# Kernel optimization log

Measured on AMD Instinct MI355X. Metric: run time of the kernel, lower is better.

## Reference

```python
import jax, jax.numpy as jnp
import numpy as np

N = 8192
D_IN = 1024
D_OUT = 1024


def setup_inputs() -> dict:
    key = jax.random.key(0)
    k0, k1, k2, k3 = jax.random.split(key, 4)
    scale = 1.0 / np.sqrt(D_IN)  # roughly matches nn.Linear init magnitude
    return {
        "x": jax.random.normal(k0, (N, D_IN), dtype=jnp.float32),
        "Wq": jax.random.normal(k1, (D_IN, D_OUT), dtype=jnp.float32) * scale,
        "Wk": jax.random.normal(k2, (D_IN, D_OUT), dtype=jnp.float32) * scale,
        "Wv": jax.random.normal(k3, (D_IN, D_OUT), dtype=jnp.float32) * scale,
    }


def reference(x, Wq, Wk, Wv):
    # QKV projections (bias-free Linear); weights stored [d_in, d_out]
    q = x @ Wq  # [N, d_out]
    k = x @ Wk  # [N, d_out]
    v = x @ Wv  # [N, d_out]
    # full N x N attention scores, scaled by sqrt(d_out), softmax over keys
    scores = jnp.einsum("nd,md->nm", q, k) / jnp.sqrt(jnp.asarray(k.shape[-1], x.dtype))
    weights = jax.nn.softmax(scores, axis=-1)
    return weights @ v  # [N, d_out]
```

## Files before the change

### kernel.cpp

```cpp
#include <hip/hip_runtime.h>
#include <hip/hip_bf16.h>
#include <stdint.h>
#include <stddef.h>

using bf16 = __hip_bfloat16;

typedef __attribute__((ext_vector_type(8))) short bf16x8;
typedef __attribute__((ext_vector_type(4))) float f32x4;

#define NROWS 8192
#define DDIM  1024

#define GLDS16(gsrc, ldst)                                                     \
  __builtin_amdgcn_global_load_lds(                                            \
      (const __attribute__((address_space(1))) uint32_t*)(gsrc),               \
      (__attribute__((address_space(3))) uint32_t*)(ldst), 16, 0, 0)

__global__ void cvt_f32_bf16_k(const float* __restrict__ in, bf16* __restrict__ out, int n) {
  int i = blockIdx.x * blockDim.x + threadIdx.x;
  int idx = i * 4;
  if (idx < n) {
    float4 v = *reinterpret_cast<const float4*>(in + idx);
    alignas(8) bf16 t[4] = {(bf16)v.x, (bf16)v.y, (bf16)v.z, (bf16)v.w};
    *reinterpret_cast<uint2*>(out + idx) = *reinterpret_cast<const uint2*>(t);
  }
}

template <typename Tin>
__global__ void transpose_bf16_k(const Tin* __restrict__ in, bf16* __restrict__ out,
                                 int R, int C) {
  __shared__ float tile[32][33];
  int bx = blockIdx.x * 32;
  int by = blockIdx.y * 32;
  int tx = threadIdx.x, ty = threadIdx.y;
#pragma unroll
  for (int i = 0; i < 32; i += 8)
    tile[ty + i][tx] = (float)in[(size_t)(by + ty + i) * C + (bx + tx)];
  __syncthreads();
#pragma unroll
  for (int i = 0; i < 32; i += 8)
    out[(size_t)(bx + ty + i) * R + (by + tx)] = (bf16)tile[tx][ty + i];
}

__global__ void rowsum_k(const bf16* __restrict__ P, float* __restrict__ Z, int Kc) {
  int lane = threadIdx.x & 63;
  int wave = threadIdx.x >> 6;
  int row = blockIdx.x * 4 + wave;
  const bf16* p = P + (size_t)row * Kc;
  float s = 0.f;
  for (int c = lane * 8; c < Kc; c += 64 * 8) {
    bf16x8 v = *reinterpret_cast<const bf16x8*>(p + c);
#pragma unroll
    for (int j = 0; j < 8; j++)
      s += __uint_as_float(((uint32_t)(uint16_t)v[j]) << 16);
  }
#pragma unroll
  for (int off = 32; off > 0; off >>= 1) s += __shfl_down(s, off);
  if (lane == 0) Z[row] = s;
}

__global__ void combine_k(const float* __restrict__ P0, const float* __restrict__ P1,
                          const float* __restrict__ Z, float* __restrict__ out, int total) {
  int i = blockIdx.x * blockDim.x + threadIdx.x;
  int idx = i * 4;
  if (idx < total) {
    float4 a = *reinterpret_cast<const float4*>(P0 + idx);
    float4 b = *reinterpret_cast<const float4*>(P1 + idx);
    float rz = 1.0f / Z[idx >> 10];
    float4 o;
    o.x = (a.x + b.x) * rz; o.y = (a.y + b.y) * rz;
    o.z = (a.z + b.z) * rz; o.w = (a.w + b.w) * rz;
    *reinterpret_cast<float4*>(out + idx) = o;
  }
}

template <int EPI>
__global__ __launch_bounds__(256) void gemm_bt_k(
    const bf16* __restrict__ A, const bf16* __restrict__ B, void* __restrict__ Cv,
    const float* __restrict__ Z, int M, int N, int K, float scale) {
  __shared__ alignas(16) bf16 As[128 * 32];
  __shared__ alignas(16) bf16 Bs[128 * 32];

  const int tid = threadIdx.x;
  const int lane = tid & 63;
  const int wave = tid >> 6;
  const int wr = (wave >> 1) * 64;
  const int wc = (wave & 1) * 64;

  const int mBase = blockIdx.y * 128;
  const int nBase = blockIdx.x * 128;

  const int srow = tid >> 2;
  const int skel = (tid & 3) * 8;

  const bf16* gA0 = A + (size_t)(mBase + srow) * K + skel;
  const bf16* gA1 = A + (size_t)(mBase + srow + 64) * K + skel;
  const bf16* gB0 = B + (size_t)(nBase + srow) * K + skel;
  const bf16* gB1 = B + (size_t)(nBase + srow + 64) * K + skel;

  bf16* lA0 = &As[srow * 32 + skel];
  bf16* lA1 = &As[(srow + 64) * 32 + skel];
  bf16* lB0 = &Bs[srow * 32 + skel];
  bf16* lB1 = &Bs[(srow + 64) * 32 + skel];

  f32x4 acc[4][4];
  f32x4 zero = {0.f, 0.f, 0.f, 0.f};
#pragma unroll
  for (int i = 0; i < 4; i++)
#pragma unroll
    for (int j = 0; j < 4; j++) acc[i][j] = zero;

  const int fr = lane & 15;
  const int fk = (lane >> 4) * 8;

  for (int k0 = 0; k0 < K; k0 += 32) {
    GLDS16(gA0 + k0, lA0);
    GLDS16(gA1 + k0, lA1);
    GLDS16(gB0 + k0, lB0);
    GLDS16(gB1 + k0, lB1);
    __syncthreads();

    bf16x8 a[4], b[4];
#pragma unroll
    for (int mi = 0; mi < 4; mi++)
      a[mi] = *reinterpret_cast<const bf16x8*>(&As[(wr + mi * 16 + fr) * 32 + fk]);
#pragma unroll
    for (int nj = 0; nj < 4; nj++)
      b[nj] = *reinterpret_cast<const bf16x8*>(&Bs[(wc + nj * 16 + fr) * 32 + fk]);
#pragma unroll
    for (int mi = 0; mi < 4; mi++)
#pragma unroll
      for (int nj = 0; nj < 4; nj++)
        acc[mi][nj] = __builtin_amdgcn_mfma_f32_16x16x32_bf16(a[mi], b[nj], acc[mi][nj], 0, 0, 0);
    __syncthreads();
  }

#pragma unroll
  for (int mi = 0; mi < 4; mi++) {
#pragma unroll
    for (int nj = 0; nj < 4; nj++) {
      int col = nBase + wc + nj * 16 + fr;
#pragma unroll
      for (int j = 0; j < 4; j++) {
        int row = mBase + wr + mi * 16 + (lane >> 4) * 4 + j;
        float v = acc[mi][nj][j];
        if (EPI == 0) {
          ((bf16*)Cv)[(size_t)row * N + col] = (bf16)(v * scale);
        }
      }
    }
  }
}

template <int EPI>
__global__ __launch_bounds__(512, 2) void gemm256_k(
    const bf16* __restrict__ A, const bf16* __restrict__ B, void* __restrict__ Cv,
    int M, int N, int K, int ksplit) {
  __shared__ alignas(1024) bf16 smem[4 * 16384];

  const int tid = threadIdx.x;
  const int lane = tid & 63;
  const int wave = tid >> 6;
  const int wm = wave >> 2;
  const int wn = wave & 3;

  const int nwgx = gridDim.x;
  const int nwg = nwgx * gridDim.y;
  const int wg = blockIdx.y * nwgx + blockIdx.x;
  const int cpx = nwg >> 3;
  const int swz = (wg & 7) * cpx + (wg >> 3);
  const int bx = swz % nwgx;
  const int by = swz / nwgx;
  const int mBase = by * 256;
  const int nBase = bx * 256;

  const int z = blockIdx.z;
  const int kbase = z * ksplit;
  const int NT = ksplit / 32;

  const int sr = lane >> 2;
  const int ssl = (lane & 3) ^ ((lane >> 3) & 3);
  const bf16* srcA0 = A + (size_t)(mBase + wave * 16 + sr) * K + kbase + ssl * 8;
  const bf16* srcA1 = A + (size_t)(mBase + (wave + 8) * 16 + sr) * K + kbase + ssl * 8;
  const bf16* srcB0 = B + (size_t)(nBase + wave * 16 + sr) * K + kbase + ssl * 8;
  const bf16* srcB1 = B + (size_t)(nBase + (wave + 8) * 16 + sr) * K + kbase + ssl * 8;

  const int fr = lane & 15;
  const int laneElem = fr * 32 + (((lane >> 4) ^ ((fr >> 1) & 3)) * 8);

  f32x4 acc[8][4];
  f32x4 zero = {0.f, 0.f, 0.f, 0.f};
#pragma unroll
  for (int m = 0; m < 8; m++)
#pragma unroll
    for (int n = 0; n < 4; n++) acc[m][n] = zero;

  auto stage = [&](int t) {
    bf16* base = smem + (t & 3) * 16384;
    int kk = t * 32;
    GLDS16(srcA0 + kk, base + wave * 512);
    GLDS16(srcA1 + kk, base + (wave + 8) * 512);
    GLDS16(srcB0 + kk, base + 8192 + wave * 512);
    GLDS16(srcB1 + kk, base + 8192 + (wave + 8) * 512);
  };

  stage(0);
  if (NT > 1) stage(1);
  if (NT > 2) stage(2);

  for (int t = 0; t < NT; ++t) {
    __builtin_amdgcn_s_barrier();
    if (t + 3 < NT) stage(t + 3);
    int infl = NT - 1 - t;
    if (infl > 3) infl = 3;
    if (infl == 3)      asm volatile("s_waitcnt vmcnt(12)" ::: "memory");
    else if (infl == 2) asm volatile("s_waitcnt vmcnt(8)" ::: "memory");
    else if (infl == 1) asm volatile("s_waitcnt vmcnt(4)" ::: "memory");
    else                asm volatile("s_waitcnt vmcnt(0)" ::: "memory");
    __builtin_amdgcn_s_barrier();

    const bf16* bufA = smem + (t & 3) * 16384;
    const bf16* bufB = bufA + 8192;
    bf16x8 a[8], b[4];
#pragma unroll
    for (int m = 0; m < 8; m++)
      a[m] = *reinterpret_cast<const bf16x8*>(bufA + (wm * 128 + m * 16) * 32 + laneElem);
#pragma unroll
    for (int n = 0; n < 4; n++)
      b[n] = *reinterpret_cast<const bf16x8*>(bufB + (wn * 64 + n * 16) * 32 + laneElem);
#pragma unroll
    for (int m = 0; m < 8; m++)
#pragma unroll
      for (int n = 0; n < 4; n++)
        acc[m][n] = __builtin_amdgcn_mfma_f32_16x16x32_bf16(a[m], b[n], acc[m][n], 0, 0, 0);
  }

#pragma unroll
  for (int m = 0; m < 8; m++) {
#pragma unroll
    for (int n = 0; n < 4; n++) {
      int col = nBase + wn * 64 + n * 16 + fr;
#pragma unroll
      for (int j = 0; j < 4; j++) {
        int row = mBase + wm * 128 + m * 16 + (lane >> 4) * 4 + j;
        float v = acc[m][n][j];
        if (EPI == 1) {
          ((bf16*)Cv)[(size_t)row * N + col] = (bf16)__expf(v);
        } else {
          float* Cp = (float*)Cv + (size_t)z * M * N;
          Cp[(size_t)row * N + col] = v;
        }
      }
    }
  }
}

extern "C" void kernel_launch(void* const* d_in, const int* in_sizes, int n_in,
                              void* d_out, int out_size, void* d_ws, size_t ws_size,
                              hipStream_t stream) {
  (void)in_sizes; (void)n_in; (void)out_size; (void)ws_size;
  const float* x  = (const float*)d_in[0];
  const float* Wq = (const float*)d_in[1];
  const float* Wk = (const float*)d_in[2];
  const float* Wv = (const float*)d_in[3];
  float* out = (float*)d_out;

  char* ws = (char*)d_ws;
  const size_t MB = 1024 * 1024;
  size_t o = 0;
  float* Z  = (float*)(ws + o); o += 64 * 1024;
  size_t xb_off = o;
  bf16* xb  = (bf16*)(ws + o); o += (size_t)NROWS * DDIM * 2;
  bf16* WqT = (bf16*)(ws + o); o += (size_t)DDIM * DDIM * 2;
  bf16* WkT = (bf16*)(ws + o); o += (size_t)DDIM * DDIM * 2;
  bf16* WvT = (bf16*)(ws + o); o += (size_t)DDIM * DDIM * 2;
  bf16* Qb  = (bf16*)(ws + o); o += (size_t)NROWS * DDIM * 2;
  bf16* Kb  = (bf16*)(ws + o); o += (size_t)NROWS * DDIM * 2;
  bf16* Vb  = (bf16*)(ws + o); o += (size_t)NROWS * DDIM * 2;
  bf16* Vt  = (bf16*)(ws + o); o += (size_t)DDIM * NROWS * 2;
  bf16* P   = (bf16*)(ws + o); o += (size_t)NROWS * NROWS * 2;
  float* Pp = (float*)(ws + xb_off);
  (void)MB;

  {
    int n = NROWS * DDIM;
    cvt_f32_bf16_k<<<(n / 4 + 255) / 256, 256, 0, stream>>>(x, xb, n);
  }
  {
    dim3 tb(32, 8);
    transpose_bf16_k<float><<<dim3(32, 32), tb, 0, stream>>>(Wq, WqT, DDIM, DDIM);
    transpose_bf16_k<float><<<dim3(32, 32), tb, 0, stream>>>(Wk, WkT, DDIM, DDIM);
    transpose_bf16_k<float><<<dim3(32, 32), tb, 0, stream>>>(Wv, WvT, DDIM, DDIM);
  }
  {
    dim3 grid(DDIM / 128, NROWS / 128);
    gemm_bt_k<0><<<grid, 256, 0, stream>>>(xb, WqT, Qb, nullptr, NROWS, DDIM, DDIM, 0.03125f);
    gemm_bt_k<0><<<grid, 256, 0, stream>>>(xb, WkT, Kb, nullptr, NROWS, DDIM, DDIM, 1.0f);
    gemm_bt_k<0><<<grid, 256, 0, stream>>>(xb, WvT, Vb, nullptr, NROWS, DDIM, DDIM, 1.0f);
  }
  {
    dim3 tb(32, 8);
    transpose_bf16_k<bf16><<<dim3(DDIM / 32, NROWS / 32), tb, 0, stream>>>(Vb, Vt, NROWS, DDIM);
  }
  gemm256_k<1><<<dim3(NROWS / 256, NROWS / 256, 1), 512, 0, stream>>>(
      Qb, Kb, P, NROWS, NROWS, DDIM, DDIM);
  rowsum_k<<<NROWS / 4, 256, 0, stream>>>(P, Z, NROWS);
  gemm256_k<3><<<dim3(DDIM / 256, NROWS / 256, 2), 512, 0, stream>>>(
      P, Vt, Pp, NROWS, DDIM, NROWS, NROWS / 2);
  {
    int total = NROWS * DDIM;
    combine_k<<<(total / 4 + 255) / 256, 256, 0, stream>>>(
        Pp, Pp + (size_t)NROWS * DDIM, Z, out, total);
  }
}
```

Measured before the change: 435.3 us.

## Restructure 256x256 GEMM into four-phase double-buffered pipeline; compute V transposed directly

The main 256x256 GEMM moves from a 4-stage K=32 buffer ring to a double-buffered K=64 tile with an XOR swizzle. Each K-step is split into four phases that interleave LDS fragment reads, global-to-LDS prefetch of the next tile, and MFMA blocks, with priority raised around the MFMAs. Separately, V is now computed directly in transposed form by swapping the GEMM operands, which removes the separate V transpose kernel and its round trip through memory. The finer-grained barriers and waitcnt bookkeeping add synchronisation overhead and the risk of subtle ordering errors.

```diff
diff --git a/kernel.cpp b/kernel.cpp
--- a/kernel.cpp
+++ b/kernel.cpp
@@ -15,6 +15,8 @@
   __builtin_amdgcn_global_load_lds(                                            \
       (const __attribute__((address_space(1))) uint32_t*)(gsrc),               \
       (__attribute__((address_space(3))) uint32_t*)(ldst), 16, 0, 0)
+
+#define MFMA16(a, b, c) __builtin_amdgcn_mfma_f32_16x16x32_bf16((a), (b), (c), 0, 0, 0)
 
 __global__ void cvt_f32_bf16_k(const float* __restrict__ in, bf16* __restrict__ out, int n) {
   int i = blockIdx.x * blockDim.x + threadIdx.x;
@@ -28,14 +30,14 @@
 
 template <typename Tin>
 __global__ void transpose_bf16_k(const Tin* __restrict__ in, bf16* __restrict__ out,
-                                 int R, int C) {
+                                 int R, int C, int ldin) {
   __shared__ float tile[32][33];
   int bx = blockIdx.x * 32;
   int by = blockIdx.y * 32;
   int tx = threadIdx.x, ty = threadIdx.y;
 #pragma unroll
   for (int i = 0; i < 32; i += 8)
-    tile[ty + i][tx] = (float)in[(size_t)(by + ty + i) * C + (bx + tx)];
+    tile[ty + i][tx] = (float)in[(size_t)(by + ty + i) * ldin + (bx + tx)];
   __syncthreads();
 #pragma unroll
   for (int i = 0; i < 32; i += 8)
@@ -77,7 +79,7 @@
 template <int EPI>
 __global__ __launch_bounds__(256) void gemm_bt_k(
     const bf16* __restrict__ A, const bf16* __restrict__ B, void* __restrict__ Cv,
-    const float* __restrict__ Z, int M, int N, int K, float scale) {
+    int M, int N, int K, float scale) {
   __shared__ alignas(16) bf16 As[128 * 32];
   __shared__ alignas(16) bf16 Bs[128 * 32];
 
@@ -156,7 +158,7 @@
 __global__ __launch_bounds__(512, 2) void gemm256_k(
     const bf16* __restrict__ A, const bf16* __restrict__ B, void* __restrict__ Cv,
     int M, int N, int K, int ksplit) {
-  __shared__ alignas(1024) bf16 smem[4 * 16384];
+  __shared__ alignas(1024) bf16 smem[2 * 32768];
 
   const int tid = threadIdx.x;
   const int lane = tid & 63;
@@ -176,17 +178,13 @@
 
   const int z = blockIdx.z;
   const int kbase = z * ksplit;
-  const int NT = ksplit / 32;
-
-  const int sr = lane >> 2;
-  const int ssl = (lane & 3) ^ ((lane >> 3) & 3);
-  const bf16* srcA0 = A + (size_t)(mBase + wave * 16 + sr) * K + kbase + ssl * 8;
-  const bf16* srcA1 = A + (size_t)(mBase + (wave + 8) * 16 + sr) * K + kbase + ssl * 8;
-  const bf16* srcB0 = B + (size_t)(nBase + wave * 16 + sr) * K + kbase + ssl * 8;
-  const bf16* srcB1 = B + (size_t)(nBase + (wave + 8) * 16 + sr) * K + kbase + ssl * 8;
+  const int NT = ksplit / 64;
+
+  const int laneRow = lane >> 3;
+  const int laneSwz = ((lane & 7) ^ laneRow) * 8;
 
   const int fr = lane & 15;
-  const int laneElem = fr * 32 + (((lane >> 4) ^ ((fr >> 1) & 3)) * 8);
+  const int kq = lane >> 4;
 
   f32x4 acc[8][4];
   f32x4 zero = {0.f, 0.f, 0.f, 0.f};
@@ -195,45 +193,129 @@
 #pragma unroll
     for (int n = 0; n < 4; n++) acc[m][n] = zero;
 
-  auto stage = [&](int t) {
-    bf16* base = smem + (t & 3) * 16384;
-    int kk = t * 32;
-    GLDS16(srcA0 + kk, base + wave * 512);
-    GLDS16(srcA1 + kk, base + (wave + 8) * 512);
-    GLDS16(srcB0 + kk, base + 8192 + wave * 512);
-    GLDS16(srcB1 + kk, base + 8192 + (wave + 8) * 512);
+  auto sg = [&](int t, int x, int r0) {
+    const bf16* src = (x == 0)
+        ? A + (size_t)(mBase + r0 + laneRow) * K + kbase + t * 64 + laneSwz
+        : B + (size_t)(nBase + r0 + laneRow) * K + kbase + t * 64 + laneSwz;
+    bf16* dst = smem + (t & 1) * 32768 + x * 16384 + r0 * 64;
+    GLDS16(src, dst);
   };
-
-  stage(0);
-  if (NT > 1) stage(1);
-  if (NT > 2) stage(2);
-
-  for (int t = 0; t < NT; ++t) {
+  auto stBh0 = [&](int t) { sg(t, 1, wave * 16);       sg(t, 1, wave * 16 + 8); };
+  auto stBh1 = [&](int t) { sg(t, 1, 128 + wave * 16); sg(t, 1, 136 + wave * 16); };
+  auto stAE  = [&](int t) { sg(t, 0, wave * 8);        sg(t, 0, 128 + wave * 8); };
+  auto stAL  = [&](int t) { sg(t, 0, 64 + wave * 8);   sg(t, 0, 192 + wave * 8); };
+
+  auto rdA = [&](const bf16* buf, int m, int ks) {
+    int row = wm * 128 + m * 16 + fr;
+    int ps = (ks * 4 + kq) ^ (row & 7);
+    return *reinterpret_cast<const bf16x8*>(buf + row * 64 + ps * 8);
+  };
+  auto rdB = [&](const bf16* buf, int n, int ks) {
+    int row = wn * 64 + n * 16 + fr;
+    int ps = (ks * 4 + kq) ^ (row & 7);
+    return *reinterpret_cast<const bf16x8*>(buf + 16384 + row * 64 + ps * 8);
+  };
+
+#define PHASE_SYNC()                                                           \
+  __builtin_amdgcn_s_barrier();                                                \
+  asm volatile("s_waitcnt lgkmcnt(0)" ::: "memory");                           \
+  __builtin_amdgcn_sched_barrier(0)
+
+  stBh0(0); stBh1(0); stAE(0); stAL(0);
+  asm volatile("s_waitcnt vmcnt(0)" ::: "memory");
+  __builtin_amdgcn_s_barrier();
+
+  for (int s = 0; s < NT; ++s) {
+    const bf16* buf = smem + (s & 1) * 32768;
+    const bool st = (s + 1 < NT);
+    bf16x8 bfr[4][2], afr[2][2];
+
+#pragma unroll
+    for (int n = 0; n < 4; n++) {
+      bfr[n][0] = rdB(buf, n, 0);
+      bfr[n][1] = rdB(buf, n, 1);
+    }
+#pragma unroll
+    for (int i = 0; i < 2; i++) {
+      afr[i][0] = rdA(buf, i, 0);
+      afr[i][1] = rdA(buf, i, 1);
+    }
+    if (st) stBh0(s + 1);
+    PHASE_SYNC();
+    __builtin_amdgcn_s_setprio(1);
+#pragma unroll
+    for (int ks = 0; ks < 2; ks++)
+#pragma unroll
+      for (int i = 0; i < 2; i++)
+#pragma unroll
+        for (int n = 0; n < 4; n++)
+          acc[i][n] = MFMA16(afr[i][ks], bfr[n][ks], acc[i][n]);
+    __builtin_amdgcn_s_setprio(0);
     __builtin_amdgcn_s_barrier();
-    if (t + 3 < NT) stage(t + 3);
-    int infl = NT - 1 - t;
-    if (infl > 3) infl = 3;
-    if (infl == 3)      asm volatile("s_waitcnt vmcnt(12)" ::: "memory");
-    else if (infl == 2) asm volatile("s_waitcnt vmcnt(8)" ::: "memory");
-    else if (infl == 1) asm volatile("s_waitcnt vmcnt(4)" ::: "memory");
-    else                asm volatile("s_waitcnt vmcnt(0)" ::: "memory");
+
+#pragma unroll
+    for (int i = 0; i < 2; i++) {
+      afr[i][0] = rdA(buf, 2 + i, 0);
+      afr[i][1] = rdA(buf, 2 + i, 1);
+    }
+    if (st) {
+      stBh1(s + 1);
+      asm volatile("s_waitcnt vmcnt(4)" ::: "memory");
+    } else {
+      asm volatile("s_waitcnt vmcnt(0)" ::: "memory");
+    }
+    PHASE_SYNC();
+    __builtin_amdgcn_s_setprio(1);
+#pragma unroll
+    for (int ks = 0; ks < 2; ks++)
+#pragma unroll
+      for (int i = 0; i < 2; i++)
+#pragma unroll
+        for (int n = 0; n < 4; n++)
+          acc[2 + i][n] = MFMA16(afr[i][ks], bfr[n][ks], acc[2 + i][n]);
+    __builtin_amdgcn_s_setprio(0);
     __builtin_amdgcn_s_barrier();
 
-    const bf16* bufA = smem + (t & 3) * 16384;
-    const bf16* bufB = bufA + 8192;
-    bf16x8 a[8], b[4];
-#pragma unroll
-    for (int m = 0; m < 8; m++)
-      a[m] = *reinterpret_cast<const bf16x8*>(bufA + (wm * 128 + m * 16) * 32 + laneElem);
-#pragma unroll
-    for (int n = 0; n < 4; n++)
-      b[n] = *reinterpret_cast<const bf16x8*>(bufB + (wn * 64 + n * 16) * 32 + laneElem);
-#pragma unroll
-    for (int m = 0; m < 8; m++)
-#pragma unroll
-      for (int n = 0; n < 4; n++)
-        acc[m][n] = __builtin_amdgcn_mfma_f32_16x16x32_bf16(a[m], b[n], acc[m][n], 0, 0, 0);
-  }
+#pragma unroll
+    for (int i = 0; i < 2; i++) {
+      afr[i][0] = rdA(buf, 4 + i, 0);
+      afr[i][1] = rdA(buf, 4 + i, 1);
+    }
+    if (st) stAE(s + 1);
+    PHASE_SYNC();
+    __builtin_amdgcn_s_setprio(1);
+#pragma unroll
+    for (int ks = 0; ks < 2; ks++)
+#pragma unroll
+      for (int i = 0; i < 2; i++)
+#pragma unroll
+        for (int n = 0; n < 4; n++)
+          acc[4 + i][n] = MFMA16(afr[i][ks], bfr[n][ks], acc[4 + i][n]);
+    __builtin_amdgcn_s_setprio(0);
+    __builtin_amdgcn_s_barrier();
+
+#pragma unroll
+    for (int i = 0; i < 2; i++) {
+      afr[i][0] = rdA(buf, 6 + i, 0);
+      afr[i][1] = rdA(buf, 6 + i, 1);
+    }
+    if (st) {
+      stAL(s + 1);
+      asm volatile("s_waitcnt vmcnt(2)" ::: "memory");
+    }
+    PHASE_SYNC();
+    __builtin_amdgcn_s_setprio(1);
+#pragma unroll
+    for (int ks = 0; ks < 2; ks++)
+#pragma unroll
+      for (int i = 0; i < 2; i++)
+#pragma unroll
+        for (int n = 0; n < 4; n++)
+          acc[6 + i][n] = MFMA16(afr[i][ks], bfr[n][ks], acc[6 + i][n]);
+    __builtin_amdgcn_s_setprio(0);
+    __builtin_amdgcn_s_barrier();
+  }
+#undef PHASE_SYNC
 
 #pragma unroll
   for (int m = 0; m < 8; m++) {
@@ -242,7 +324,7 @@
       int col = nBase + wn * 64 + n * 16 + fr;
 #pragma unroll
       for (int j = 0; j < 4; j++) {
-        int row = mBase + wm * 128 + m * 16 + (lane >> 4) * 4 + j;
+        int row = mBase + wm * 128 + m * 16 + kq * 4 + j;
         float v = acc[m][n][j];
         if (EPI == 1) {
           ((bf16*)Cv)[(size_t)row * N + col] = (bf16)__expf(v);
@@ -266,9 +348,8 @@
   float* out = (float*)d_out;
 
   char* ws = (char*)d_ws;
-  const size_t MB = 1024 * 1024;
   size_t o = 0;
-  float* Z  = (float*)(ws + o); o += 64 * 1024;
+  float* Z   = (float*)(ws + o); o += 64 * 1024;
   size_t xb_off = o;
   bf16* xb  = (bf16*)(ws + o); o += (size_t)NROWS * DDIM * 2;
   bf16* WqT = (bf16*)(ws + o); o += (size_t)DDIM * DDIM * 2;
@@ -276,11 +357,11 @@
   bf16* WvT = (bf16*)(ws + o); o += (size_t)DDIM * DDIM * 2;
   bf16* Qb  = (bf16*)(ws + o); o += (size_t)NROWS * DDIM * 2;
   bf16* Kb  = (bf16*)(ws + o); o += (size_t)NROWS * DDIM * 2;
-  bf16* Vb  = (bf16*)(ws + o); o += (size_t)NROWS * DDIM * 2;
+  bf16* Vsp = (bf16*)(ws + o); o += (size_t)NROWS * DDIM * 2;
   bf16* Vt  = (bf16*)(ws + o); o += (size_t)DDIM * NROWS * 2;
   bf16* P   = (bf16*)(ws + o); o += (size_t)NROWS * NROWS * 2;
   float* Pp = (float*)(ws + xb_off);
-  (void)MB;
+  (void)Vsp;
 
   {
     int n = NROWS * DDIM;
@@ -288,19 +369,16 @@
   }
   {
     dim3 tb(32, 8);
-    transpose_bf16_k<float><<<dim3(32, 32), tb, 0, stream>>>(Wq, WqT, DDIM, DDIM);
-    transpose_bf16_k<float><<<dim3(32, 32), tb, 0, stream>>>(Wk, WkT, DDIM, DDIM);
-    transpose_bf16_k<float><<<dim3(32, 32), tb, 0, stream>>>(Wv, WvT, DDIM, DDIM);
+    transpose_bf16_k<float><<<dim3(32, 32), tb, 0, stream>>>(Wq, WqT, DDIM, DDIM, DDIM);
+    transpose_bf16_k<float><<<dim3(32, 32), tb, 0, stream>>>(Wk, WkT, DDIM, DDIM, DDIM);
+    transpose_bf16_k<float><<<dim3(32, 32), tb, 0, stream>>>(Wv, WvT, DDIM, DDIM, DDIM);
   }
   {
     dim3 grid(DDIM / 128, NROWS / 128);
-    gemm_bt_k<0><<<grid, 256, 0, stream>>>(xb, WqT, Qb, nullptr, NROWS, DDIM, DDIM, 0.03125f);
-    gemm_bt_k<0><<<grid, 256, 0, stream>>>(xb, WkT, Kb, nullptr, NROWS, DDIM, DDIM, 1.0f);
-    gemm_bt_k<0><<<grid, 256, 0, stream>>>(xb, WvT, Vb, nullptr, NROWS, DDIM, DDIM, 1.0f);
-  }
-  {
-    dim3 tb(32, 8);
-    transpose_bf16_k<bf16><<<dim3(DDIM / 32, NROWS / 32), tb, 0, stream>>>(Vb, Vt, NROWS, DDIM);
+    gemm_bt_k<0><<<grid, 256, 0, stream>>>(xb, WqT, Qb, NROWS, DDIM, DDIM, 0.03125f);
+    gemm_bt_k<0><<<grid, 256, 0, stream>>>(xb, WkT, Kb, NROWS, DDIM, DDIM, 1.0f);
+    gemm_bt_k<0><<<dim3(NROWS / 128, DDIM / 128), 256, 0, stream>>>(
+        WvT, xb, Vt, DDIM, NROWS, DDIM, 1.0f);
   }
   gemm256_k<1><<<dim3(NROWS / 256, NROWS / 256, 1), 512, 0, stream>>>(
       Qb, Kb, P, NROWS, NROWS, DDIM, DDIM);
```

After: 413.8 us. 4.9% less time.

## Split gemm256 main loop into two phases and compute V transposed directly

Applied to the files above, without the earlier changes.

The 256-tile GEMM loop is restructured into two half-phases. Each phase issues half of the next stage's global-to-LDS loads, reads half of the A fragments, and runs 16 MFMAs under raised wave priority. Per-phase barriers with tuned vmcnt waits aim to overlap LDS reads, global prefetch and matrix math better. Separately, V^T is produced directly by swapping the operands of the projection GEMM (WvT x xb), which removes the separate V transpose kernel and its memory round trip.

```diff
diff --git a/kernel.cpp b/kernel.cpp
--- a/kernel.cpp
+++ b/kernel.cpp
@@ -15,6 +15,8 @@
   __builtin_amdgcn_global_load_lds(                                            \
       (const __attribute__((address_space(1))) uint32_t*)(gsrc),               \
       (__attribute__((address_space(3))) uint32_t*)(ldst), 16, 0, 0)
+
+#define MFMA16(a, b, c) __builtin_amdgcn_mfma_f32_16x16x32_bf16((a), (b), (c), 0, 0, 0)
 
 __global__ void cvt_f32_bf16_k(const float* __restrict__ in, bf16* __restrict__ out, int n) {
   int i = blockIdx.x * blockDim.x + threadIdx.x;
@@ -28,14 +30,14 @@
 
 template <typename Tin>
 __global__ void transpose_bf16_k(const Tin* __restrict__ in, bf16* __restrict__ out,
-                                 int R, int C) {
+                                 int R, int C, int ldin) {
   __shared__ float tile[32][33];
   int bx = blockIdx.x * 32;
   int by = blockIdx.y * 32;
   int tx = threadIdx.x, ty = threadIdx.y;
 #pragma unroll
   for (int i = 0; i < 32; i += 8)
-    tile[ty + i][tx] = (float)in[(size_t)(by + ty + i) * C + (bx + tx)];
+    tile[ty + i][tx] = (float)in[(size_t)(by + ty + i) * ldin + (bx + tx)];
   __syncthreads();
 #pragma unroll
   for (int i = 0; i < 32; i += 8)
@@ -77,7 +79,7 @@
 template <int EPI>
 __global__ __launch_bounds__(256) void gemm_bt_k(
     const bf16* __restrict__ A, const bf16* __restrict__ B, void* __restrict__ Cv,
-    const float* __restrict__ Z, int M, int N, int K, float scale) {
+    int M, int N, int K, float scale) {
   __shared__ alignas(16) bf16 As[128 * 32];
   __shared__ alignas(16) bf16 Bs[128 * 32];
 
@@ -195,45 +197,77 @@
 #pragma unroll
     for (int n = 0; n < 4; n++) acc[m][n] = zero;
 
-  auto stage = [&](int t) {
+  auto stageH0 = [&](int t) {
     bf16* base = smem + (t & 3) * 16384;
     int kk = t * 32;
     GLDS16(srcA0 + kk, base + wave * 512);
     GLDS16(srcA1 + kk, base + (wave + 8) * 512);
+  };
+  auto stageH1 = [&](int t) {
+    bf16* base = smem + (t & 3) * 16384;
+    int kk = t * 32;
     GLDS16(srcB0 + kk, base + 8192 + wave * 512);
     GLDS16(srcB1 + kk, base + 8192 + (wave + 8) * 512);
   };
-
-  stage(0);
-  if (NT > 1) stage(1);
-  if (NT > 2) stage(2);
+  auto rdA = [&](const bf16* buf, int m) {
+    return *reinterpret_cast<const bf16x8*>(buf + (wm * 128 + m * 16) * 32 + laneElem);
+  };
+  auto rdB = [&](const bf16* buf, int n) {
+    return *reinterpret_cast<const bf16x8*>(buf + 8192 + (wn * 64 + n * 16) * 32 + laneElem);
+  };
+
+#define PHASE_SYNC()                                                           \
+  __builtin_amdgcn_s_barrier();                                                \
+  asm volatile("s_waitcnt lgkmcnt(0)" ::: "memory");                           \
+  __builtin_amdgcn_sched_barrier(0)
+
+  stageH0(0); stageH1(0);
+  stageH0(1); stageH1(1);
+  stageH0(2); stageH1(2);
+  asm volatile("s_waitcnt vmcnt(8)" ::: "memory");
+  __builtin_amdgcn_s_barrier();
 
   for (int t = 0; t < NT; ++t) {
+    const bf16* buf = smem + (t & 3) * 16384;
+    const bool st = (t + 3 < NT);
+    bf16x8 bfr[4], afr[4];
+
+#pragma unroll
+    for (int n = 0; n < 4; n++) bfr[n] = rdB(buf, n);
+#pragma unroll
+    for (int m = 0; m < 4; m++) afr[m] = rdA(buf, m);
+    if (st) stageH0(t + 3);
+    PHASE_SYNC();
+    __builtin_amdgcn_s_setprio(1);
+#pragma unroll
+    for (int m = 0; m < 4; m++)
+#pragma unroll
+      for (int n = 0; n < 4; n++)
+        acc[m][n] = MFMA16(afr[m], bfr[n], acc[m][n]);
+    __builtin_amdgcn_s_setprio(0);
     __builtin_amdgcn_s_barrier();
-    if (t + 3 < NT) stage(t + 3);
-    int infl = NT - 1 - t;
-    if (infl > 3) infl = 3;
-    if (infl == 3)      asm volatile("s_waitcnt vmcnt(12)" ::: "memory");
-    else if (infl == 2) asm volatile("s_waitcnt vmcnt(8)" ::: "memory");
-    else if (infl == 1) asm volatile("s_waitcnt vmcnt(4)" ::: "memory");
-    else                asm volatile("s_waitcnt vmcnt(0)" ::: "memory");
+
+#pragma unroll
+    for (int m = 0; m < 4; m++) afr[m] = rdA(buf, m + 4);
+    if (st) stageH1(t + 3);
+    if (t + 1 < NT) {
+      int hi = (t + 3 < NT) ? (t + 3) : (NT - 1);
+      int slack = hi - (t + 1);
+      if (slack >= 2)      asm volatile("s_waitcnt vmcnt(8)" ::: "memory");
+      else if (slack == 1) asm volatile("s_waitcnt vmcnt(4)" ::: "memory");
+      else                 asm volatile("s_waitcnt vmcnt(0)" ::: "memory");
+    }
+    PHASE_SYNC();
+    __builtin_amdgcn_s_setprio(1);
+#pragma unroll
+    for (int m = 0; m < 4; m++)
+#pragma unroll
+      for (int n = 0; n < 4; n++)
+        acc[m + 4][n] = MFMA16(afr[m], bfr[n], acc[m + 4][n]);
+    __builtin_amdgcn_s_setprio(0);
     __builtin_amdgcn_s_barrier();
-
-    const bf16* bufA = smem + (t & 3) * 16384;
-    const bf16* bufB = bufA + 8192;
-    bf16x8 a[8], b[4];
-#pragma unroll
-    for (int m = 0; m < 8; m++)
-      a[m] = *reinterpret_cast<const bf16x8*>(bufA + (wm * 128 + m * 16) * 32 + laneElem);
-#pragma unroll
-    for (int n = 0; n < 4; n++)
-      b[n] = *reinterpret_cast<const bf16x8*>(bufB + (wn * 64 + n * 16) * 32 + laneElem);
-#pragma unroll
-    for (int m = 0; m < 8; m++)
-#pragma unroll
-      for (int n = 0; n < 4; n++)
-        acc[m][n] = __builtin_amdgcn_mfma_f32_16x16x32_bf16(a[m], b[n], acc[m][n], 0, 0, 0);
-  }
+  }
+#undef PHASE_SYNC
 
 #pragma unroll
   for (int m = 0; m < 8; m++) {
@@ -266,9 +300,8 @@
   float* out = (float*)d_out;
 
   char* ws = (char*)d_ws;
-  const size_t MB = 1024 * 1024;
   size_t o = 0;
-  float* Z  = (float*)(ws + o); o += 64 * 1024;
+  float* Z   = (float*)(ws + o); o += 64 * 1024;
   size_t xb_off = o;
   bf16* xb  = (bf16*)(ws + o); o += (size_t)NROWS * DDIM * 2;
   bf16* WqT = (bf16*)(ws + o); o += (size_t)DDIM * DDIM * 2;
@@ -276,11 +309,11 @@
   bf16* WvT = (bf16*)(ws + o); o += (size_t)DDIM * DDIM * 2;
   bf16* Qb  = (bf16*)(ws + o); o += (size_t)NROWS * DDIM * 2;
   bf16* Kb  = (bf16*)(ws + o); o += (size_t)NROWS * DDIM * 2;
-  bf16* Vb  = (bf16*)(ws + o); o += (size_t)NROWS * DDIM * 2;
+  bf16* Vsp = (bf16*)(ws + o); o += (size_t)NROWS * DDIM * 2;
   bf16* Vt  = (bf16*)(ws + o); o += (size_t)DDIM * NROWS * 2;
   bf16* P   = (bf16*)(ws + o); o += (size_t)NROWS * NROWS * 2;
   float* Pp = (float*)(ws + xb_off);
-  (void)MB;
+  (void)Vsp;
 
   {
     int n = NROWS * DDIM;
@@ -288,19 +321,16 @@
   }
   {
     dim3 tb(32, 8);
-    transpose_bf16_k<float><<<dim3(32, 32), tb, 0, stream>>>(Wq, WqT, DDIM, DDIM);
-    transpose_bf16_k<float><<<dim3(32, 32), tb, 0, stream>>>(Wk, WkT, DDIM, DDIM);
-    transpose_bf16_k<float><<<dim3(32, 32), tb, 0, stream>>>(Wv, WvT, DDIM, DDIM);
+    transpose_bf16_k<float><<<dim3(32, 32), tb, 0, stream>>>(Wq, WqT, DDIM, DDIM, DDIM);
+    transpose_bf16_k<float><<<dim3(32, 32), tb, 0, stream>>>(Wk, WkT, DDIM, DDIM, DDIM);
+    transpose_bf16_k<float><<<dim3(32, 32), tb, 0, stream>>>(Wv, WvT, DDIM, DDIM, DDIM);
   }
   {
     dim3 grid(DDIM / 128, NROWS / 128);
-    gemm_bt_k<0><<<grid, 256, 0, stream>>>(xb, WqT, Qb, nullptr, NROWS, DDIM, DDIM, 0.03125f);
-    gemm_bt_k<0><<<grid, 256, 0, stream>>>(xb, WkT, Kb, nullptr, NROWS, DDIM, DDIM, 1.0f);
-    gemm_bt_k<0><<<grid, 256, 0, stream>>>(xb, WvT, Vb, nullptr, NROWS, DDIM, DDIM, 1.0f);
-  }
-  {
-    dim3 tb(32, 8);
-    transpose_bf16_k<bf16><<<dim3(DDIM / 32, NROWS / 32), tb, 0, stream>>>(Vb, Vt, NROWS, DDIM);
+    gemm_bt_k<0><<<grid, 256, 0, stream>>>(xb, WqT, Qb, NROWS, DDIM, DDIM, 0.03125f);
+    gemm_bt_k<0><<<grid, 256, 0, stream>>>(xb, WkT, Kb, NROWS, DDIM, DDIM, 1.0f);
+    gemm_bt_k<0><<<dim3(NROWS / 128, DDIM / 128), 256, 0, stream>>>(
+        WvT, xb, Vt, DDIM, NROWS, DDIM, 1.0f);
   }
   gemm256_k<1><<<dim3(NROWS / 256, NROWS / 256, 1), 512, 0, stream>>>(
       Qb, Kb, P, NROWS, NROWS, DDIM, DDIM);
```

Result: faster. 418.5 us (-3.8%).
